# Kernel tuning notes

Measured on AMD Instinct MI355X. Metric: run time of the kernel, lower is better.

## Reference

```python
import jax, jax.numpy as jnp
import numpy as np

N, H = 1024, 12
SQK, SV, PQK, PV = 16, 16, 4, 8
C1, C2, COUT = 384, 128, 384


def setup_inputs() -> dict:
    key = jax.random.key(0)
    ks = jax.random.split(key, 12)
    inputs_1d = jax.random.normal(ks[0], (N, C1), jnp.float32)
    inputs_2d = jax.random.normal(ks[1], (N, N, C2), jnp.float32)
    mask = jnp.ones((N, 1), jnp.float32)
    # proper-ish rigid frames: orthonormal rotations via batched QR
    rot = jnp.linalg.qr(jax.random.normal(ks[2], (N, 3, 3), jnp.float32))[0]
    trans = jax.random.normal(ks[3], (N, 3), jnp.float32)
    s = 0.02
    params = dict(
        w_q_scalar=jax.random.normal(ks[4], (C1, H * SQK), jnp.float32) * s,
        b_q_scalar=jnp.zeros((H * SQK,), jnp.float32),
        w_kv_scalar=jax.random.normal(ks[5], (C1, H * (SQK + SV)), jnp.float32) * s,
        b_kv_scalar=jnp.zeros((H * (SQK + SV),), jnp.float32),
        w_q_point=jax.random.normal(ks[6], (C1, H * 3 * PQK), jnp.float32) * s,
        b_q_point=jnp.zeros((H * 3 * PQK,), jnp.float32),
        w_kv_point=jax.random.normal(ks[7], (C1, H * 3 * (PQK + PV)), jnp.float32) * s,
        b_kv_point=jnp.zeros((H * 3 * (PQK + PV),), jnp.float32),
        w_2d=jax.random.normal(ks[8], (C2, H), jnp.float32) * s,
        b_2d=jnp.zeros((H,), jnp.float32),
        tpw=jnp.ones((H,), jnp.float32),
        w_out=jax.random.normal(ks[9], (H * (C2 + SV + 4 * PV), COUT), jnp.float32) * s,
        b_out=jnp.zeros((COUT,), jnp.float32),
    )
    return dict(inputs_1d=inputs_1d, inputs_2d=inputs_2d, mask=mask, rot=rot, trans=trans, **params)


def _forward(inputs_1d, inputs_2d, mask, rot, trans,
             w_q_scalar, b_q_scalar, w_kv_scalar, b_kv_scalar,
             w_q_point, b_q_point, w_kv_point, b_kv_point,
             w_2d, b_2d, tpw, w_out, b_out):
    n = inputs_1d.shape[0]
    scalar_w = (1.0 / (3 * SQK)) ** 0.5            # sqrt(1/(3*scalar_variance))
    point_w = (1.0 / (3 * PQK * 4.5)) ** 0.5       # sqrt(1/(3*point_variance))
    w2d_scale = (1.0 / 3.0) ** 0.5

    q_scalar = (inputs_1d @ w_q_scalar + b_q_scalar).reshape(n, H, SQK)
    kv_scalar = (inputs_1d @ w_kv_scalar + b_kv_scalar).reshape(n, H, SQK + SV)
    k_scalar, v_scalar = kv_scalar[..., :SQK], kv_scalar[..., SQK:]

    def to_global(flat, p):
        # flat: [n, 3*H*p] split into x,y,z chunks (matches torch split order)
        pts = jnp.stack(jnp.split(flat, 3, axis=-1), axis=-1)   # [n, H*p, 3]
        g = jnp.einsum('nij,npj->npi', rot, pts) + trans[:, None, :]
        return g.reshape(n, H, p, 3)

    q_pt = to_global(inputs_1d @ w_q_point + b_q_point, PQK)            # [n,H,PQK,3]
    kv_pt = to_global(inputs_1d @ w_kv_point + b_kv_point, PQK + PV)
    k_pt, v_pt = kv_pt[:, :, :PQK], kv_pt[:, :, PQK:]

    pw = jax.nn.softplus(tpw) * point_w                                 # [H]
    qp = q_pt.transpose(1, 0, 2, 3)                                     # [H,n,PQK,3]
    kp = k_pt.transpose(1, 0, 2, 3)
    # -0.5*w_h*sum_p |q-k|^2 expanded as q2+k2-2qk to avoid [H,n,n,PQK,3] temp
    q2 = jnp.sum(qp * qp, axis=(-1, -2))                                # [H,n]
    k2 = jnp.sum(kp * kp, axis=(-1, -2))
    cross = jnp.einsum('hnpc,hmpc->hnm', qp, kp)
    attn_qk_point = -0.5 * pw[:, None, None] * (q2[:, :, None] + k2[:, None, :] - 2.0 * cross)

    attn_qk_scalar = jnp.einsum('hnc,hmc->hnm',
                                scalar_w * q_scalar.transpose(1, 0, 2),
                                k_scalar.transpose(1, 0, 2))
    a2d = (inputs_2d @ w_2d + b_2d).transpose(2, 0, 1)                  # [H,n,n]
    logits = attn_qk_scalar + attn_qk_point + a2d * w2d_scale
    mask_2d = mask * mask.T                                             # [n,n]
    logits = logits - 1e5 * (1.0 - mask_2d)
    attn = jax.nn.softmax(logits, axis=-1)                              # [H,n,n]

    res_scalar = jnp.einsum('hnm,hmc->nhc', attn, v_scalar.transpose(1, 0, 2)).reshape(n, H * SV)
    vp = v_pt.transpose(1, 0, 2, 3)                                     # [H,n,PV,3]
    res_pt_g = jnp.einsum('hnm,hmpc->nhpc', attn, vp).reshape(n, H * PV, 3)
    # invert_point: local = R^T (global - t)
    res_pt_l = jnp.einsum('nji,npj->npi', rot, res_pt_g - trans[:, None, :])
    dist = jnp.sqrt(1e-8 + jnp.sum(res_pt_l * res_pt_l, axis=-1))       # [n, H*PV]
    attn_2d = jnp.einsum('hnm,nmc->nhc', attn, inputs_2d).reshape(n, H * C2)

    final = jnp.concatenate([res_scalar, res_pt_l[..., 0], res_pt_l[..., 1],
                             res_pt_l[..., 2], dist, attn_2d], axis=-1)  # [n, 2112]
    return final @ w_out + b_out


def reference(inputs_1d, inputs_2d, mask, rot, trans,
              w_q_scalar, b_q_scalar, w_kv_scalar, b_kv_scalar,
              w_q_point, b_q_point, w_kv_point, b_kv_point,
              w_2d, b_2d, tpw, w_out, b_out):
    return _forward(inputs_1d, inputs_2d, mask, rot, trans,
                    w_q_scalar, b_q_scalar, w_kv_scalar, b_kv_scalar,
                    w_q_point, b_q_point, w_kv_point, b_kv_point,
                    w_2d, b_2d, tpw, w_out, b_out)
```

## Files before the change

### kernel.cpp

```cpp
#include <hip/hip_runtime.h>
#include <hip/hip_bf16.h>
#include <cstddef>

#define NN 1024
#define HH 12
#define SQK 16
#define SV 16
#define PQK 4
#define PV 8
#define C1 384
#define C2 128
#define COUT 384

#define HSQK (HH*SQK)
#define HKV  (HH*(SQK+SV))
#define QPF  (HH*3*PQK)
#define KVPF (HH*3*(PQK+PV))
#define FDIM (HH*(C2+SV+4*PV))

__device__ __constant__ const float SCALAR_W  = 0.14433756729740643f;
__device__ __constant__ const float POINT_W   = 0.13608276348795434f;
__device__ __constant__ const float W2D_SCALE = 0.5773502691896258f;

constexpr size_t OFF_QS     = 0;
constexpr size_t OFF_KVS    = OFF_QS     + 196608;
constexpr size_t OFF_QPF    = OFF_KVS    + 393216;
constexpr size_t OFF_KVPF   = OFF_QPF    + 147456;
constexpr size_t OFF_QPTG   = OFF_KVPF   + 442368;
constexpr size_t OFF_KVPTG  = OFF_QPTG   + 147456;
constexpr size_t OFF_Q2     = OFF_KVPTG  + 442368;
constexpr size_t OFF_K2     = OFF_Q2     + 12288;
constexpr size_t OFF_PW     = OFF_K2     + 12288;
constexpr size_t OFF_VT     = OFF_PW     + 64;
constexpr size_t OFF_RESPTG = OFF_VT     + 491520;
constexpr size_t OFF_FINAL  = OFF_RESPTG + 294912;
constexpr size_t OFF_LOGITS = OFF_FINAL  + 2162688;

template <bool ATOMIC>
__device__ void gemm_tile_128x64(const float* __restrict__ A, const float* __restrict__ W,
                                 const float* __restrict__ bias, float* __restrict__ C,
                                 int K, int Ncols, int m0, int n0, int k0, int ktiles,
                                 bool addbias)
{
    __shared__ float As[16][136];
    __shared__ float Bs[16][68];
    const int t  = threadIdx.x;
    const int tx = t & 15;
    const int ty = t >> 4;

    float acc[8][4];
#pragma unroll
    for (int i = 0; i < 8; ++i)
#pragma unroll
        for (int j = 0; j < 4; ++j) acc[i][j] = 0.f;

    for (int kt = 0; kt < ktiles; ++kt) {
        const int kb = k0 + kt * 16;
        {
            const int mi = t >> 1, k8 = (t & 1) * 8;
            const float* src = A + (size_t)(m0 + mi) * K + kb + k8;
            float4 v0 = *(const float4*)(src);
            float4 v1 = *(const float4*)(src + 4);
            As[k8 + 0][mi] = v0.x; As[k8 + 1][mi] = v0.y;
            As[k8 + 2][mi] = v0.z; As[k8 + 3][mi] = v0.w;
            As[k8 + 4][mi] = v1.x; As[k8 + 5][mi] = v1.y;
            As[k8 + 6][mi] = v1.z; As[k8 + 7][mi] = v1.w;
        }
        {
            const int kk = t >> 4, n4 = (t & 15) * 4;
            const int col = n0 + n4;
            float4 v = make_float4(0.f, 0.f, 0.f, 0.f);
            if (col < Ncols) v = *(const float4*)(W + (size_t)(kb + kk) * Ncols + col);
            *(float4*)&Bs[kk][n4] = v;
        }
        __syncthreads();
#pragma unroll
        for (int kk = 0; kk < 16; ++kk) {
            float bv[4];
            *(float4*)bv = *(const float4*)&Bs[kk][tx * 4];
            float av[8];
            *(float4*)&av[0] = *(const float4*)&As[kk][ty * 8];
            *(float4*)&av[4] = *(const float4*)&As[kk][ty * 8 + 4];
#pragma unroll
            for (int i = 0; i < 8; ++i)
#pragma unroll
                for (int j = 0; j < 4; ++j) acc[i][j] += av[i] * bv[j];
        }
        __syncthreads();
    }
#pragma unroll
    for (int i = 0; i < 8; ++i) {
        const int row = m0 + ty * 8 + i;
#pragma unroll
        for (int j = 0; j < 4; ++j) {
            const int col = n0 + tx * 4 + j;
            if (col < Ncols) {
                float v = acc[i][j] + (addbias ? bias[col] : 0.f);
                if (ATOMIC) atomicAdd(&C[(size_t)row * Ncols + col], v);
                else        C[(size_t)row * Ncols + col] = v;
            }
        }
    }
}

__global__ __launch_bounds__(256) void proj_kernel(
    const float* __restrict__ A,
    const float* __restrict__ wqs,  const float* __restrict__ bqs,
    const float* __restrict__ wkvs, const float* __restrict__ bkvs,
    const float* __restrict__ wqp,  const float* __restrict__ bqp,
    const float* __restrict__ wkvp, const float* __restrict__ bkvp,
    float* __restrict__ qs, float* __restrict__ kvs,
    float* __restrict__ qpf, float* __restrict__ kvpf)
{
    const int ct = blockIdx.x % 19;
    const int mt = blockIdx.x / 19;
    const float *W, *bias; float* C; int Ncols, n0;
    if (ct < 3)       { W = wqs;  bias = bqs;  C = qs;   Ncols = 192; n0 = ct * 64; }
    else if (ct < 9)  { W = wkvs; bias = bkvs; C = kvs;  Ncols = 384; n0 = (ct - 3) * 64; }
    else if (ct < 12) { W = wqp;  bias = bqp;  C = qpf;  Ncols = 144; n0 = (ct - 9) * 64; }
    else              { W = wkvp; bias = bkvp; C = kvpf; Ncols = 432; n0 = (ct - 12) * 64; }
    gemm_tile_128x64<false>(A, W, bias, C, C1, Ncols, mt * 128, n0, 0, 24, true);
}

__global__ __launch_bounds__(192) void points_kernel(
    const float* __restrict__ qpf, const float* __restrict__ kvpf,
    const float* __restrict__ rot, const float* __restrict__ trans,
    const float* __restrict__ tpw,
    float* __restrict__ qptg, float* __restrict__ kvptg,
    float* __restrict__ q2, float* __restrict__ k2, float* __restrict__ pw)
{
    __shared__ float lq[48 * 3];
    __shared__ float lkv[144 * 3];
    const int n = blockIdx.x, t = threadIdx.x;
    float r[9], tr[3];
#pragma unroll
    for (int i = 0; i < 9; ++i) r[i] = rot[n * 9 + i];
#pragma unroll
    for (int i = 0; i < 3; ++i) tr[i] = trans[n * 3 + i];

    if (t < 48) {
        float p0 = qpf[n * QPF + t], p1 = qpf[n * QPF + 48 + t], p2 = qpf[n * QPF + 96 + t];
#pragma unroll
        for (int i = 0; i < 3; ++i)
            lq[t * 3 + i] = r[i * 3 + 0] * p0 + r[i * 3 + 1] * p1 + r[i * 3 + 2] * p2 + tr[i];
    }
    if (t < 144) {
        float p0 = kvpf[(size_t)n * KVPF + t];
        float p1 = kvpf[(size_t)n * KVPF + 144 + t];
        float p2 = kvpf[(size_t)n * KVPF + 288 + t];
#pragma unroll
        for (int i = 0; i < 3; ++i)
            lkv[t * 3 + i] = r[i * 3 + 0] * p0 + r[i * 3 + 1] * p1 + r[i * 3 + 2] * p2 + tr[i];
    }
    __syncthreads();
    if (t < 48) {
#pragma unroll
        for (int i = 0; i < 3; ++i) qptg[(size_t)n * QPF + t * 3 + i] = lq[t * 3 + i];
    }
    if (t < 144) {
#pragma unroll
        for (int i = 0; i < 3; ++i) kvptg[(size_t)n * KVPF + t * 3 + i] = lkv[t * 3 + i];
    }
    if (t < HH) {
        float s = 0.f;
#pragma unroll
        for (int p = 0; p < 4; ++p)
#pragma unroll
            for (int i = 0; i < 3; ++i) { float v = lq[(t * 4 + p) * 3 + i]; s += v * v; }
        q2[t * NN + n] = s;
        float s2 = 0.f;
#pragma unroll
        for (int p = 0; p < 4; ++p)
#pragma unroll
            for (int i = 0; i < 3; ++i) { float v = lkv[(t * 12 + p) * 3 + i]; s2 += v * v; }
        k2[t * NN + n] = s2;
        if (n == 0) {
            float x = tpw[t];
            float sp = (x > 20.f) ? x : log1pf(__expf(x));
            pw[t] = sp * POINT_W;
        }
    }
}

__global__ __launch_bounds__(256) void vt_kernel(const float* __restrict__ kvs,
                                                 const float* __restrict__ kvptg,
                                                 float* __restrict__ vT)
{
    const int idx = blockIdx.x * 256 + threadIdx.x;
    const int r = idx >> 10, m = idx & 1023;
    float val;
    if (r < 192) {
        const int h = r >> 4, c = r & 15;
        val = kvs[(size_t)m * HKV + h * 32 + 16 + c];
    } else {
        const int q = r - 192;
        const int h = q / 24, rem = q % 24;
        val = kvptg[(size_t)m * KVPF + h * 36 + 12 + rem];
    }
    vT[(size_t)r * NN + m] = val;
}

__global__ __launch_bounds__(256) void logits_kernel(
    const float* __restrict__ in2d, const float* __restrict__ w2d, const float* __restrict__ b2d,
    const float* __restrict__ qs, const float* __restrict__ kvs,
    const float* __restrict__ qptg, const float* __restrict__ kvptg,
    const float* __restrict__ q2, const float* __restrict__ k2,
    const float* __restrict__ pw, const float* __restrict__ mask,
    float* __restrict__ logits)
{
    __shared__ float w2s[C2 * HH];
    const int t = threadIdx.x;
    for (int i = t; i < C2 * HH; i += 256) w2s[i] = w2d[i];
    __syncthreads();

    const int n = blockIdx.x >> 2;
    const int m = ((blockIdx.x & 3) << 8) + t;

    const float4* row = (const float4*)(in2d + ((size_t)n * NN + m) * C2);
    float a2[HH];
#pragma unroll
    for (int h = 0; h < HH; ++h) a2[h] = 0.f;
    for (int c4 = 0; c4 < C2 / 4; ++c4) {
        float4 v = row[c4];
        const float* w = &w2s[c4 * 4 * HH];
#pragma unroll
        for (int h = 0; h < HH; ++h)
            a2[h] += v.x * w[h] + v.y * w[HH + h] + v.z * w[2 * HH + h] + v.w * w[3 * HH + h];
    }
    const float mval = -100000.f * (1.f - mask[n] * mask[m]);
    const float* qbase = qs + (size_t)n * HSQK;
    const float* kbase = kvs + (size_t)m * HKV;
    const float* qpb = qptg + (size_t)n * QPF;
    const float* kpb = kvptg + (size_t)m * KVPF;

    for (int h = 0; h < HH; ++h) {
        const float4* qq = (const float4*)(qbase + h * SQK);
        const float4* kq = (const float4*)(kbase + h * (SQK + SV));
        float sd = 0.f;
#pragma unroll
        for (int j = 0; j < 4; ++j) {
            float4 a = qq[j], b = kq[j];
            sd += a.x * b.x + a.y * b.y + a.z * b.z + a.w * b.w;
        }
        const float4* qp = (const float4*)(qpb + h * 3 * PQK);
        const float4* kp = (const float4*)(kpb + h * 3 * (PQK + PV));
        float cr = 0.f;
#pragma unroll
        for (int j = 0; j < 3; ++j) {
            float4 a = qp[j], b = kp[j];
            cr += a.x * b.x + a.y * b.y + a.z * b.z + a.w * b.w;
        }
        float pt = -0.5f * pw[h] * (q2[h * NN + n] + k2[h * NN + m] - 2.f * cr);
        float lg = SCALAR_W * sd + pt + W2D_SCALE * (a2[h] + b2d[h]) + mval;
        logits[((size_t)h * NN + n) * NN + m] = lg;
    }
}

__global__ __launch_bounds__(256) void softmax_kernel(float* __restrict__ logits)
{
    const size_t rowid = blockIdx.x;
    float* p = logits + rowid * NN;
    const int t = threadIdx.x;
    float4 v = ((float4*)p)[t];
    float mx = fmaxf(fmaxf(v.x, v.y), fmaxf(v.z, v.w));
#pragma unroll
    for (int o = 32; o; o >>= 1) mx = fmaxf(mx, __shfl_xor(mx, o));
    __shared__ float redm[4];
    __shared__ float reds[4];
    const int w = t >> 6, lane = t & 63;
    if (lane == 0) redm[w] = mx;
    __syncthreads();
    mx = fmaxf(fmaxf(redm[0], redm[1]), fmaxf(redm[2], redm[3]));
    float e0 = __expf(v.x - mx), e1 = __expf(v.y - mx), e2 = __expf(v.z - mx), e3 = __expf(v.w - mx);
    float s = e0 + e1 + e2 + e3;
#pragma unroll
    for (int o = 32; o; o >>= 1) s += __shfl_xor(s, o);
    if (lane == 0) reds[w] = s;
    __syncthreads();
    s = reds[0] + reds[1] + reds[2] + reds[3];
    const float inv = 1.f / s;
    ((float4*)p)[t] = make_float4(e0 * inv, e1 * inv, e2 * inv, e3 * inv);
}

__global__ __launch_bounds__(256) void attn2d_kernel(
    const float* __restrict__ attn, const float* __restrict__ in2d, float* __restrict__ fin)
{
    __shared__ float la[NN * HH];
    const int t = threadIdx.x;
    const int n = blockIdx.x;
#pragma unroll
    for (int h = 0; h < HH; ++h)
#pragma unroll
        for (int k = 0; k < 4; ++k) {
            const int m = t + (k << 8);
            la[m * HH + h] = attn[((size_t)h * NN + n) * NN + m];
        }
    __syncthreads();

    const int c0 = t & 31;
    const int ml = t >> 5;
    float acc[HH][4];
#pragma unroll
    for (int h = 0; h < HH; ++h)
#pragma unroll
        for (int j = 0; j < 4; ++j) acc[h][j] = 0.f;

    const float* base = in2d + (size_t)n * NN * C2;
    for (int m = ml; m < NN; m += 8) {
        const float* r2 = base + (size_t)m * C2;
        float v0 = r2[c0], v1 = r2[c0 + 32], v2 = r2[c0 + 64], v3 = r2[c0 + 96];
        const float* am = &la[m * HH];
        float av[HH];
        *(float4*)&av[0] = *(const float4*)(am);
        *(float4*)&av[4] = *(const float4*)(am + 4);
        *(float4*)&av[8] = *(const float4*)(am + 8);
#pragma unroll
        for (int h = 0; h < HH; ++h) {
            acc[h][0] += av[h] * v0; acc[h][1] += av[h] * v1;
            acc[h][2] += av[h] * v2; acc[h][3] += av[h] * v3;
        }
    }
    for (int h = 0; h < HH; ++h) {
        __syncthreads();
        la[(ml << 7) + c0]      = acc[h][0];
        la[(ml << 7) + c0 + 32] = acc[h][1];
        la[(ml << 7) + c0 + 64] = acc[h][2];
        la[(ml << 7) + c0 + 96] = acc[h][3];
        __syncthreads();
        if (t < 128) {
            float s = 0.f;
#pragma unroll
            for (int l = 0; l < 8; ++l) s += la[(l << 7) + t];
            fin[(size_t)n * FDIM + 576 + (h << 7) + t] = s;
        }
    }
}

__global__ __launch_bounds__(256) void attnv_kernel(
    const float* __restrict__ attn, const float* __restrict__ vT,
    float* __restrict__ fin, float* __restrict__ resptg)
{
    __shared__ float la[HH * 1040];
    const int t = threadIdx.x;
    const int n = blockIdx.x;
#pragma unroll
    for (int h = 0; h < HH; ++h)
#pragma unroll
        for (int k = 0; k < 4; ++k) {
            const int m = t + (k << 8);
            la[h * 1040 + m] = attn[((size_t)h * NN + n) * NN + m];
        }
    __syncthreads();
    for (int r = t; r < 480; r += 256) {
        const int h = (r < 192) ? (r >> 4) : ((r - 192) / 24);
        const float4* vr = (const float4*)(vT + (size_t)r * NN);
        const float4* ar = (const float4*)&la[h * 1040];
        float s = 0.f;
        for (int q = 0; q < NN / 4; ++q) {
            float4 a = ar[q], v = vr[q];
            s += a.x * v.x + a.y * v.y + a.z * v.z + a.w * v.w;
        }
        if (r < 192) fin[(size_t)n * FDIM + r] = s;
        else         resptg[(size_t)n * 288 + (r - 192)] = s;
    }
}

__global__ __launch_bounds__(128) void ptout_kernel(
    const float* __restrict__ resptg, const float* __restrict__ rot,
    const float* __restrict__ trans, float* __restrict__ fin)
{
    const int n = blockIdx.x, t = threadIdx.x;
    if (t >= 96) return;
    float g0 = resptg[(size_t)n * 288 + t * 3 + 0];
    float g1 = resptg[(size_t)n * 288 + t * 3 + 1];
    float g2 = resptg[(size_t)n * 288 + t * 3 + 2];
    float d0 = g0 - trans[n * 3 + 0];
    float d1 = g1 - trans[n * 3 + 1];
    float d2 = g2 - trans[n * 3 + 2];
    float l0 = rot[n * 9 + 0] * d0 + rot[n * 9 + 3] * d1 + rot[n * 9 + 6] * d2;
    float l1 = rot[n * 9 + 1] * d0 + rot[n * 9 + 4] * d1 + rot[n * 9 + 7] * d2;
    float l2 = rot[n * 9 + 2] * d0 + rot[n * 9 + 5] * d1 + rot[n * 9 + 8] * d2;
    const size_t base = (size_t)n * FDIM;
    fin[base + 192 + t] = l0;
    fin[base + 288 + t] = l1;
    fin[base + 384 + t] = l2;
    fin[base + 480 + t] = sqrtf(1e-8f + l0 * l0 + l1 * l1 + l2 * l2);
}

__global__ __launch_bounds__(256) void outgemm_kernel(
    const float* __restrict__ fin, const float* __restrict__ wout,
    const float* __restrict__ bout, float* __restrict__ out)
{
    const int n0 = blockIdx.x * 64;
    const int m0 = blockIdx.y * 128;
    const int z  = blockIdx.z;
    gemm_tile_128x64<true>(fin, wout, bout, out, FDIM, COUT, m0, n0, z * 352, 22, z == 0);
}

extern "C" void kernel_launch(void* const* d_in, const int* in_sizes, int n_in,
                              void* d_out, int out_size, void* d_ws, size_t ws_size,
                              hipStream_t stream)
{
    const float* in1d  = (const float*)d_in[0];
    const float* in2d  = (const float*)d_in[1];
    const float* mask  = (const float*)d_in[2];
    const float* rot   = (const float*)d_in[3];
    const float* trans = (const float*)d_in[4];
    const float* wqs   = (const float*)d_in[5];
    const float* bqs   = (const float*)d_in[6];
    const float* wkvs  = (const float*)d_in[7];
    const float* bkvs  = (const float*)d_in[8];
    const float* wqp   = (const float*)d_in[9];
    const float* bqp   = (const float*)d_in[10];
    const float* bkvpW = (const float*)d_in[11];
    const float* bkvpB = (const float*)d_in[12];
    const float* w2d   = (const float*)d_in[13];
    const float* b2d   = (const float*)d_in[14];
    const float* tpw   = (const float*)d_in[15];
    const float* wout  = (const float*)d_in[16];
    const float* bout  = (const float*)d_in[17];

    float* ws     = (float*)d_ws;
    float* qs     = ws + OFF_QS;
    float* kvs    = ws + OFF_KVS;
    float* qpf    = ws + OFF_QPF;
    float* kvpf   = ws + OFF_KVPF;
    float* qptg   = ws + OFF_QPTG;
    float* kvptg  = ws + OFF_KVPTG;
    float* q2     = ws + OFF_Q2;
    float* k2     = ws + OFF_K2;
    float* pw     = ws + OFF_PW;
    float* vT     = ws + OFF_VT;
    float* resptg = ws + OFF_RESPTG;
    float* fin    = ws + OFF_FINAL;
    float* logits = ws + OFF_LOGITS;

    hipMemsetAsync(d_out, 0, (size_t)out_size * sizeof(float), stream);

    proj_kernel<<<152, 256, 0, stream>>>(in1d, wqs, bqs, wkvs, bkvs, wqp, bqp, bkvpW, bkvpB,
                                         qs, kvs, qpf, kvpf);
    points_kernel<<<NN, 192, 0, stream>>>(qpf, kvpf, rot, trans, tpw, qptg, kvptg, q2, k2, pw);
    vt_kernel<<<1920, 256, 0, stream>>>(kvs, kvptg, vT);
    logits_kernel<<<4096, 256, 0, stream>>>(in2d, w2d, b2d, qs, kvs, qptg, kvptg,
                                            q2, k2, pw, mask, logits);
    softmax_kernel<<<HH * NN, 256, 0, stream>>>(logits);
    attn2d_kernel<<<NN, 256, 0, stream>>>(logits, in2d, fin);
    attnv_kernel<<<NN, 256, 0, stream>>>(logits, vT, fin, resptg);
    ptout_kernel<<<NN, 128, 0, stream>>>(resptg, rot, trans, fin);
    outgemm_kernel<<<dim3(6, 8, 6), 256, 0, stream>>>(fin, wout, bout, (float*)d_out);
}
```

Measured before the change: 1.426 ms.

## Split logits into QK GEMM-like pass and fused 2D-bias plus softmax kernel

Result: slower. 1.773 ms (+24.3%).

```diff
diff --git a/kernel.cpp b/kernel.cpp
--- a/kernel.cpp
+++ b/kernel.cpp
@@ -34,7 +34,7 @@
 constexpr size_t OFF_VT     = OFF_PW     + 64;
 constexpr size_t OFF_RESPTG = OFF_VT     + 491520;
 constexpr size_t OFF_FINAL  = OFF_RESPTG + 294912;
-constexpr size_t OFF_LOGITS = OFF_FINAL  + 2162688;
+constexpr size_t OFF_BASE   = OFF_FINAL  + 2162688;
 
 template <bool ATOMIC>
 __device__ void gemm_tile_128x64(const float* __restrict__ A, const float* __restrict__ W,
@@ -182,157 +182,222 @@
     }
 }
 
-__global__ __launch_bounds__(256) void vt_kernel(const float* __restrict__ kvs,
-                                                 const float* __restrict__ kvptg,
-                                                 float* __restrict__ vT)
-{
-    const int idx = blockIdx.x * 256 + threadIdx.x;
-    const int r = idx >> 10, m = idx & 1023;
-    float val;
-    if (r < 192) {
-        const int h = r >> 4, c = r & 15;
-        val = kvs[(size_t)m * HKV + h * 32 + 16 + c];
+__global__ __launch_bounds__(256) void tables_kernel(const float* __restrict__ kvs,
+                                                     const float* __restrict__ kvptg,
+                                                     float* __restrict__ vT,
+                                                     float* __restrict__ kt2)
+{
+    const int b = blockIdx.x, t = threadIdx.x;
+    if (b < NN) {
+        const int m = b;
+        for (int o = t; o < 480; o += 256) {
+            float val;
+            if (o < 192) {
+                const int h = o >> 4, c = o & 15;
+                val = kvs[(size_t)m * HKV + h * 32 + 16 + c];
+            } else {
+                const int q = o - 192, h = q / 24, j = q % 24;
+                val = kvptg[(size_t)m * KVPF + h * 36 + 12 + j];
+            }
+            vT[(size_t)m * 480 + o] = val;
+        }
     } else {
-        const int q = r - 192;
-        const int h = q / 24, rem = q % 24;
-        val = kvptg[(size_t)m * KVPF + h * 36 + 12 + rem];
-    }
-    vT[(size_t)r * NN + m] = val;
-}
-
-__global__ __launch_bounds__(256) void logits_kernel(
-    const float* __restrict__ in2d, const float* __restrict__ w2d, const float* __restrict__ b2d,
-    const float* __restrict__ qs, const float* __restrict__ kvs,
-    const float* __restrict__ qptg, const float* __restrict__ kvptg,
-    const float* __restrict__ q2, const float* __restrict__ k2,
-    const float* __restrict__ pw, const float* __restrict__ mask,
-    float* __restrict__ logits)
-{
-    __shared__ float w2s[C2 * HH];
+        const int i = (b - NN) * 256 + t;
+        const int m = i & 1023, hf = i >> 10;
+        if (hf < 336) {
+            const int h = hf / 28, f = hf % 28;
+            float val = (f < 16) ? kvs[(size_t)m * HKV + h * 32 + f]
+                                 : kvptg[(size_t)m * KVPF + h * 36 + (f - 16)];
+            kt2[(size_t)hf * NN + m] = val;
+        }
+    }
+}
+
+__global__ __launch_bounds__(256) void qkbase_kernel(
+    const float* __restrict__ qs, const float* __restrict__ qptg,
+    const float* __restrict__ kt2, const float* __restrict__ q2,
+    const float* __restrict__ k2, const float* __restrict__ pw,
+    const float* __restrict__ mask, const float* __restrict__ b2d,
+    float* __restrict__ base)
+{
+    __shared__ float qf[8 * 28];
+    __shared__ float q2s[8];
+    __shared__ float mks[8];
+    const int h = blockIdx.x >> 7;
+    const int n0 = (blockIdx.x & 127) * 8;
     const int t = threadIdx.x;
-    for (int i = t; i < C2 * HH; i += 256) w2s[i] = w2d[i];
-    __syncthreads();
-
-    const int n = blockIdx.x >> 2;
-    const int m = ((blockIdx.x & 3) << 8) + t;
-
-    const float4* row = (const float4*)(in2d + ((size_t)n * NN + m) * C2);
-    float a2[HH];
-#pragma unroll
-    for (int h = 0; h < HH; ++h) a2[h] = 0.f;
-    for (int c4 = 0; c4 < C2 / 4; ++c4) {
-        float4 v = row[c4];
-        const float* w = &w2s[c4 * 4 * HH];
+    const float pwh = pw[h];
+
+    if (t < 224) {
+        const int ni = t / 28, f = t % 28;
+        float v = (f < 16) ? SCALAR_W * qs[(size_t)(n0 + ni) * HSQK + h * 16 + f]
+                           : pwh * qptg[(size_t)(n0 + ni) * QPF + h * 12 + (f - 16)];
+        qf[t] = v;
+    }
+    if (t < 8) { q2s[t] = q2[h * NN + n0 + t]; mks[t] = mask[n0 + t]; }
+    __syncthreads();
+
+    const int m4 = t * 4;
+    float4 acc[8];
+#pragma unroll
+    for (int ni = 0; ni < 8; ++ni) acc[ni] = make_float4(0.f, 0.f, 0.f, 0.f);
+
+    for (int f = 0; f < 28; ++f) {
+        float4 kv = *(const float4*)(kt2 + ((size_t)(h * 28 + f)) * NN + m4);
+#pragma unroll
+        for (int ni = 0; ni < 8; ++ni) {
+            float s = qf[ni * 28 + f];
+            acc[ni].x += s * kv.x; acc[ni].y += s * kv.y;
+            acc[ni].z += s * kv.z; acc[ni].w += s * kv.w;
+        }
+    }
+    float4 k2v = *(const float4*)(k2 + h * NN + m4);
+    float4 mm  = *(const float4*)(mask + m4);
+    const float bb = W2D_SCALE * b2d[h];
+#pragma unroll
+    for (int ni = 0; ni < 8; ++ni) {
+        float4 o;
+        const float q2n = q2s[ni], mkn = mks[ni];
+        o.x = acc[ni].x - 0.5f * pwh * (q2n + k2v.x) + bb - 100000.f * (1.f - mkn * mm.x);
+        o.y = acc[ni].y - 0.5f * pwh * (q2n + k2v.y) + bb - 100000.f * (1.f - mkn * mm.y);
+        o.z = acc[ni].z - 0.5f * pwh * (q2n + k2v.z) + bb - 100000.f * (1.f - mkn * mm.z);
+        o.w = acc[ni].w - 0.5f * pwh * (q2n + k2v.w) + bb - 100000.f * (1.f - mkn * mm.w);
+        *(float4*)(base + ((size_t)h * NN + n0 + ni) * NN + m4) = o;
+    }
+}
+
+__global__ __launch_bounds__(256) void a2dsm_kernel(
+    const float* __restrict__ in2d, const float* __restrict__ w2d,
+    float* __restrict__ base )
+{
+    __shared__ float lg[12 * 1040];
+    __shared__ float ws2[C2 * HH];
+    const int n = blockIdx.x, t = threadIdx.x;
+
+    for (int i = t; i < C2 * HH; i += 256) ws2[i] = w2d[i];
+#pragma unroll
+    for (int h = 0; h < HH; ++h) {
+        float4 v = *(const float4*)(base + ((size_t)h * NN + n) * NN + 4 * t);
+        *(float4*)&lg[h * 1040 + 4 * t] = v;
+    }
+    __syncthreads();
+
+    const int c4 = t & 31;
+    float wreg[4][12];
+#pragma unroll
+    for (int i = 0; i < 4; ++i)
 #pragma unroll
         for (int h = 0; h < HH; ++h)
-            a2[h] += v.x * w[h] + v.y * w[HH + h] + v.z * w[2 * HH + h] + v.w * w[3 * HH + h];
-    }
-    const float mval = -100000.f * (1.f - mask[n] * mask[m]);
-    const float* qbase = qs + (size_t)n * HSQK;
-    const float* kbase = kvs + (size_t)m * HKV;
-    const float* qpb = qptg + (size_t)n * QPF;
-    const float* kpb = kvptg + (size_t)m * KVPF;
-
-    for (int h = 0; h < HH; ++h) {
-        const float4* qq = (const float4*)(qbase + h * SQK);
-        const float4* kq = (const float4*)(kbase + h * (SQK + SV));
-        float sd = 0.f;
-#pragma unroll
-        for (int j = 0; j < 4; ++j) {
-            float4 a = qq[j], b = kq[j];
-            sd += a.x * b.x + a.y * b.y + a.z * b.z + a.w * b.w;
-        }
-        const float4* qp = (const float4*)(qpb + h * 3 * PQK);
-        const float4* kp = (const float4*)(kpb + h * 3 * (PQK + PV));
-        float cr = 0.f;
-#pragma unroll
-        for (int j = 0; j < 3; ++j) {
-            float4 a = qp[j], b = kp[j];
-            cr += a.x * b.x + a.y * b.y + a.z * b.z + a.w * b.w;
-        }
-        float pt = -0.5f * pw[h] * (q2[h * NN + n] + k2[h * NN + m] - 2.f * cr);
-        float lg = SCALAR_W * sd + pt + W2D_SCALE * (a2[h] + b2d[h]) + mval;
-        logits[((size_t)h * NN + n) * NN + m] = lg;
-    }
-}
-
-__global__ __launch_bounds__(256) void softmax_kernel(float* __restrict__ logits)
-{
-    const size_t rowid = blockIdx.x;
-    float* p = logits + rowid * NN;
-    const int t = threadIdx.x;
-    float4 v = ((float4*)p)[t];
-    float mx = fmaxf(fmaxf(v.x, v.y), fmaxf(v.z, v.w));
-#pragma unroll
-    for (int o = 32; o; o >>= 1) mx = fmaxf(mx, __shfl_xor(mx, o));
-    __shared__ float redm[4];
-    __shared__ float reds[4];
-    const int w = t >> 6, lane = t & 63;
-    if (lane == 0) redm[w] = mx;
-    __syncthreads();
-    mx = fmaxf(fmaxf(redm[0], redm[1]), fmaxf(redm[2], redm[3]));
-    float e0 = __expf(v.x - mx), e1 = __expf(v.y - mx), e2 = __expf(v.z - mx), e3 = __expf(v.w - mx);
-    float s = e0 + e1 + e2 + e3;
-#pragma unroll
-    for (int o = 32; o; o >>= 1) s += __shfl_xor(s, o);
-    if (lane == 0) reds[w] = s;
-    __syncthreads();
-    s = reds[0] + reds[1] + reds[2] + reds[3];
-    const float inv = 1.f / s;
-    ((float4*)p)[t] = make_float4(e0 * inv, e1 * inv, e2 * inv, e3 * inv);
+            wreg[i][h] = W2D_SCALE * ws2[(c4 * 4 + i) * HH + h];
+
+    const int rgrp = t >> 5;
+    const int b1 = t & 1, b2 = (t >> 1) & 1;
+    const bool writer = ((t & 28) == 0);
+    const int hbase = 6 * b1 + 3 * b2;
+    const float* src = in2d + ((size_t)n * NN) * C2 + c4 * 4;
+
+    for (int j = 0; j < 128; ++j) {
+        const int row = j * 8 + rgrp;
+        float4 v = *(const float4*)(src + (size_t)row * C2);
+        float part[12];
+#pragma unroll
+        for (int h = 0; h < HH; ++h)
+            part[h] = v.x * wreg[0][h] + v.y * wreg[1][h] + v.z * wreg[2][h] + v.w * wreg[3][h];
+        float s6[6];
+#pragma unroll
+        for (int k = 0; k < 6; ++k) {
+            float keep = b1 ? part[k + 6] : part[k];
+            float give = b1 ? part[k] : part[k + 6];
+            s6[k] = keep + __shfl_xor(give, 1);
+        }
+        float s3[3];
+#pragma unroll
+        for (int k = 0; k < 3; ++k) {
+            float keep = b2 ? s6[k + 3] : s6[k];
+            float give = b2 ? s6[k] : s6[k + 3];
+            s3[k] = keep + __shfl_xor(give, 2);
+        }
+#pragma unroll
+        for (int k = 0; k < 3; ++k) {
+            s3[k] += __shfl_xor(s3[k], 4);
+            s3[k] += __shfl_xor(s3[k], 8);
+            s3[k] += __shfl_xor(s3[k], 16);
+        }
+        if (writer) {
+#pragma unroll
+            for (int k = 0; k < 3; ++k)
+                lg[(hbase + k) * 1040 + row] += s3[k];
+        }
+    }
+    __syncthreads();
+
+    const int w = t >> 6, l = t & 63;
+#pragma unroll
+    for (int k = 0; k < 3; ++k) {
+        const int h = w * 3 + k;
+        float e[16];
+        float mx = -3.0e38f;
+#pragma unroll
+        for (int i = 0; i < 16; ++i) { e[i] = lg[h * 1040 + i * 64 + l]; mx = fmaxf(mx, e[i]); }
+#pragma unroll
+        for (int o = 1; o <= 32; o <<= 1) mx = fmaxf(mx, __shfl_xor(mx, o));
+        float s = 0.f;
+#pragma unroll
+        for (int i = 0; i < 16; ++i) { e[i] = __expf(e[i] - mx); s += e[i]; }
+#pragma unroll
+        for (int o = 1; o <= 32; o <<= 1) s += __shfl_xor(s, o);
+        const float inv = 1.f / s;
+        float* dst = base + ((size_t)h * NN + n) * NN;
+#pragma unroll
+        for (int i = 0; i < 16; ++i) dst[i * 64 + l] = e[i] * inv;
+    }
 }
 
 __global__ __launch_bounds__(256) void attn2d_kernel(
     const float* __restrict__ attn, const float* __restrict__ in2d, float* __restrict__ fin)
 {
-    __shared__ float la[NN * HH];
-    const int t = threadIdx.x;
-    const int n = blockIdx.x;
+    __shared__ float sh[13200];
+    const int n = blockIdx.x, t = threadIdx.x;
+#pragma unroll
+    for (int h = 0; h < HH; ++h) {
+        float4 v = *(const float4*)(attn + ((size_t)h * NN + n) * NN + 4 * t);
+        *(float4*)&sh[h * 1040 + 4 * t] = v;
+    }
+    __syncthreads();
+
+    const int c4 = t & 31, rgrp = t >> 5;
+    float acc[12][4];
 #pragma unroll
     for (int h = 0; h < HH; ++h)
 #pragma unroll
-        for (int k = 0; k < 4; ++k) {
-            const int m = t + (k << 8);
-            la[m * HH + h] = attn[((size_t)h * NN + n) * NN + m];
-        }
-    __syncthreads();
-
-    const int c0 = t & 31;
-    const int ml = t >> 5;
-    float acc[HH][4];
+        for (int i = 0; i < 4; ++i) acc[h][i] = 0.f;
+
+    const float* src = in2d + ((size_t)n * NN) * C2 + c4 * 4;
+    for (int j = 0; j < 128; ++j) {
+        const int row = j * 8 + rgrp;
+        float4 v = *(const float4*)(src + (size_t)row * C2);
+        float p[12];
+#pragma unroll
+        for (int h = 0; h < HH; ++h) p[h] = sh[h * 1040 + row];
+#pragma unroll
+        for (int h = 0; h < HH; ++h) {
+            acc[h][0] += p[h] * v.x; acc[h][1] += p[h] * v.y;
+            acc[h][2] += p[h] * v.z; acc[h][3] += p[h] * v.w;
+        }
+    }
+    __syncthreads();
 #pragma unroll
     for (int h = 0; h < HH; ++h)
-#pragma unroll
-        for (int j = 0; j < 4; ++j) acc[h][j] = 0.f;
-
-    const float* base = in2d + (size_t)n * NN * C2;
-    for (int m = ml; m < NN; m += 8) {
-        const float* r2 = base + (size_t)m * C2;
-        float v0 = r2[c0], v1 = r2[c0 + 32], v2 = r2[c0 + 64], v3 = r2[c0 + 96];
-        const float* am = &la[m * HH];
-        float av[HH];
-        *(float4*)&av[0] = *(const float4*)(am);
-        *(float4*)&av[4] = *(const float4*)(am + 4);
-        *(float4*)&av[8] = *(const float4*)(am + 8);
-#pragma unroll
-        for (int h = 0; h < HH; ++h) {
-            acc[h][0] += av[h] * v0; acc[h][1] += av[h] * v1;
-            acc[h][2] += av[h] * v2; acc[h][3] += av[h] * v3;
-        }
-    }
-    for (int h = 0; h < HH; ++h) {
-        __syncthreads();
-        la[(ml << 7) + c0]      = acc[h][0];
-        la[(ml << 7) + c0 + 32] = acc[h][1];
-        la[(ml << 7) + c0 + 64] = acc[h][2];
-        la[(ml << 7) + c0 + 96] = acc[h][3];
-        __syncthreads();
-        if (t < 128) {
-            float s = 0.f;
-#pragma unroll
-            for (int l = 0; l < 8; ++l) s += la[(l << 7) + t];
-            fin[(size_t)n * FDIM + 576 + (h << 7) + t] = s;
-        }
+        *(float4*)&sh[(rgrp * 12 + h) * 132 + c4 * 4] = *(float4*)&acc[h][0];
+    __syncthreads();
+#pragma unroll
+    for (int u = 0; u < 6; ++u) {
+        const int o = t + 256 * u;
+        const int h = o >> 7, c = o & 127;
+        float s = 0.f;
+#pragma unroll
+        for (int g = 0; g < 8; ++g) s += sh[(g * 12 + h) * 132 + c];
+        fin[(size_t)n * FDIM + 576 + o] = s;
     }
 }
 
@@ -340,29 +405,32 @@
     const float* __restrict__ attn, const float* __restrict__ vT,
     float* __restrict__ fin, float* __restrict__ resptg)
 {
-    __shared__ float la[HH * 1040];
-    const int t = threadIdx.x;
-    const int n = blockIdx.x;
-#pragma unroll
-    for (int h = 0; h < HH; ++h)
-#pragma unroll
-        for (int k = 0; k < 4; ++k) {
-            const int m = t + (k << 8);
-            la[h * 1040 + m] = attn[((size_t)h * NN + n) * NN + m];
-        }
-    __syncthreads();
-    for (int r = t; r < 480; r += 256) {
-        const int h = (r < 192) ? (r >> 4) : ((r - 192) / 24);
-        const float4* vr = (const float4*)(vT + (size_t)r * NN);
-        const float4* ar = (const float4*)&la[h * 1040];
-        float s = 0.f;
-        for (int q = 0; q < NN / 4; ++q) {
-            float4 a = ar[q], v = vr[q];
-            s += a.x * v.x + a.y * v.y + a.z * v.z + a.w * v.w;
-        }
-        if (r < 192) fin[(size_t)n * FDIM + r] = s;
-        else         resptg[(size_t)n * 288 + (r - 192)] = s;
-    }
+    __shared__ float p17[NN * 17];
+    const int n = blockIdx.x, t = threadIdx.x;
+#pragma unroll
+    for (int h = 0; h < HH; ++h) {
+        float4 v = *(const float4*)(attn + ((size_t)h * NN + n) * NN + 4 * t);
+        p17[(4 * t + 0) * 17 + h] = v.x;
+        p17[(4 * t + 1) * 17 + h] = v.y;
+        p17[(4 * t + 2) * 17 + h] = v.z;
+        p17[(4 * t + 3) * 17 + h] = v.w;
+    }
+    __syncthreads();
+
+    const int o1 = t;
+    const int o2 = 256 + t;
+    const int h1 = (o1 < 192) ? (o1 >> 4) : (o1 - 192) / 24;
+    const int h2 = (o2 - 192) / 24;
+    const bool has2 = (t < 224);
+    float a1 = 0.f, a2 = 0.f;
+    for (int m = 0; m < NN; ++m) {
+        const float* vr = vT + (size_t)m * 480;
+        a1 += p17[m * 17 + h1] * vr[o1];
+        if (has2) a2 += p17[m * 17 + h2] * vr[o2];
+    }
+    if (o1 < 192) fin[(size_t)n * FDIM + o1] = a1;
+    else          resptg[(size_t)n * 288 + (o1 - 192)] = a1;
+    if (has2)     resptg[(size_t)n * 288 + (o2 - 192)] = a2;
 }
 
 __global__ __launch_bounds__(128) void ptout_kernel(
@@ -412,8 +480,8 @@
     const float* bkvs  = (const float*)d_in[8];
     const float* wqp   = (const float*)d_in[9];
     const float* bqp   = (const float*)d_in[10];
-    const float* bkvpW = (const float*)d_in[11];
-    const float* bkvpB = (const float*)d_in[12];
+    const float* wkvp  = (const float*)d_in[11];
+    const float* bkvp  = (const float*)d_in[12];
     const float* w2d   = (const float*)d_in[13];
     const float* b2d   = (const float*)d_in[14];
     const float* tpw   = (const float*)d_in[15];
@@ -425,6 +493,7 @@
     float* kvs    = ws + OFF_KVS;
     float* qpf    = ws + OFF_QPF;
     float* kvpf   = ws + OFF_KVPF;
+    float* kt2    = ws + OFF_KVPF;
     float* qptg   = ws + OFF_QPTG;
     float* kvptg  = ws + OFF_KVPTG;
     float* q2     = ws + OFF_Q2;
@@ -433,19 +502,18 @@
     float* vT     = ws + OFF_VT;
     float* resptg = ws + OFF_RESPTG;
     float* fin    = ws + OFF_FINAL;
-    float* logits = ws + OFF_LOGITS;
+    float* base   = ws + OFF_BASE;
 
     hipMemsetAsync(d_out, 0, (size_t)out_size * sizeof(float), stream);
 
-    proj_kernel<<<152, 256, 0, stream>>>(in1d, wqs, bqs, wkvs, bkvs, wqp, bqp, bkvpW, bkvpB,
+    proj_kernel<<<152, 256, 0, stream>>>(in1d, wqs, bqs, wkvs, bkvs, wqp, bqp, wkvp, bkvp,
                                          qs, kvs, qpf, kvpf);
     points_kernel<<<NN, 192, 0, stream>>>(qpf, kvpf, rot, trans, tpw, qptg, kvptg, q2, k2, pw);
-    vt_kernel<<<1920, 256, 0, stream>>>(kvs, kvptg, vT);
-    logits_kernel<<<4096, 256, 0, stream>>>(in2d, w2d, b2d, qs, kvs, qptg, kvptg,
-                                            q2, k2, pw, mask, logits);
-    softmax_kernel<<<HH * NN, 256, 0, stream>>>(logits);
-    attn2d_kernel<<<NN, 256, 0, stream>>>(logits, in2d, fin);
-    attnv_kernel<<<NN, 256, 0, stream>>>(logits, vT, fin, resptg);
+    tables_kernel<<<NN + 1344, 256, 0, stream>>>(kvs, kvptg, vT, kt2);
+    qkbase_kernel<<<12 * 128, 256, 0, stream>>>(qs, qptg, kt2, q2, k2, pw, mask, b2d, base);
+    a2dsm_kernel<<<NN, 256, 0, stream>>>(in2d, w2d, base);
+    attn2d_kernel<<<NN, 256, 0, stream>>>(base, in2d, fin);
+    attnv_kernel<<<NN, 256, 0, stream>>>(base, vT, fin, resptg);
     ptout_kernel<<<NN, 128, 0, stream>>>(resptg, rot, trans, fin);
     outgemm_kernel<<<dim3(6, 8, 6), 256, 0, stream>>>(fin, wout, bout, (float*)d_out);
 }
```
